# Kernel tuning notes

Hardware: AMD Instinct MI355X
Metric: run time of the kernel (lower is better)

Reference implementation:

```python
import jax, jax.numpy as jnp
import numpy as np

H, K, D = 24, 2, 128          # query heads, kv heads, head_size
HIDDEN = H * D                # 3072
ROPE_THETA = 10000.0


def setup_inputs() -> dict:
    key = jax.random.key(0)
    ks = jax.random.split(key, 6)
    B, S = 2, 2048
    T = B * S
    hidden_states = jax.random.normal(ks[0], (T, HIDDEN), dtype=jnp.float32)
    w_qkv = jax.random.normal(ks[1], ((H + 2 * K) * D, HIDDEN), dtype=jnp.float32) * (HIDDEN ** -0.5)
    b_qkv = jax.random.normal(ks[2], ((H + 2 * K) * D,), dtype=jnp.float32) * 0.02
    w_o = jax.random.normal(ks[3], (HIDDEN, H * D), dtype=jnp.float32) * (HIDDEN ** -0.5)
    b_o = jax.random.normal(ks[4], (HIDDEN,), dtype=jnp.float32) * 0.02
    # rotary tables: positions restart per sequence (flash-varlen prefill layout)
    pos = jnp.tile(jnp.arange(S, dtype=jnp.float32), B)            # [T]
    inv_freq = 1.0 / (ROPE_THETA ** (jnp.arange(0, D, 2, dtype=jnp.float32) / D))  # [D/2]
    freqs = pos[:, None] * inv_freq[None, :]                        # [T, D/2]
    return {
        "hidden_states": hidden_states,
        "w_qkv": w_qkv, "b_qkv": b_qkv,
        "w_o": w_o, "b_o": b_o,
        "cos": jnp.cos(freqs), "sin": jnp.sin(freqs),
        "seq_len": S, "window": 1024,
    }


def _rope(x, cos, sin):
    # rotate-half (neox) style, as in TGI PositionRotaryEmbedding
    half = x.shape[-1] // 2
    x1, x2 = x[..., :half], x[..., half:]
    c, s = cos[:, None, :], sin[:, None, :]   # broadcast over head dim
    return jnp.concatenate([x1 * c - x2 * s, x2 * c + x1 * s], axis=-1)


def reference(hidden_states, w_qkv, b_qkv, w_o, b_o, cos, sin, seq_len, window):
    T = hidden_states.shape[0]
    B = T // seq_len
    scale = D ** -0.5

    # fused QKV projection
    qkv = hidden_states @ w_qkv.T + b_qkv                 # [T, (H+2K)*D]
    q = qkv[:, : H * D].reshape(T, H, D)
    kv = qkv[:, H * D:].reshape(T, 2, K, D)
    k, v = kv[:, 0], kv[:, 1]                             # [T, K, D]

    q = _rope(q, cos, sin)
    k = _rope(k, cos, sin)

    # GQA: expand kv heads to query heads
    groups = H // K
    qb = q.reshape(B, seq_len, H, D)
    kb = jnp.repeat(k.reshape(B, seq_len, K, D), groups, axis=2)  # [B,S,H,D]
    vb = jnp.repeat(v.reshape(B, seq_len, K, D), groups, axis=2)

    scores = jnp.einsum("bqhd,bkhd->bhqk", qb, kb) * scale        # [B,H,S,S]
    idx = jnp.arange(seq_len)
    delta = idx[:, None] - idx[None, :]
    mask = (delta >= 0) & (delta < window)                        # causal + sliding window
    scores = jnp.where(mask[None, None], scores, jnp.float32(-1e9))
    attn = jax.nn.softmax(scores, axis=-1)
    out = jnp.einsum("bhqk,bkhd->bqhd", attn, vb).reshape(T, H * D)
    return out @ w_o.T + b_o
```

## Files before the change

### kernel.cpp

```cpp
#include <hip/hip_runtime.h>
#include <hip/hip_bf16.h>

typedef __attribute__((ext_vector_type(8))) short bf16x8;
typedef __attribute__((ext_vector_type(4))) float f32x4;

__device__ __forceinline__ short f2bf_bits(float f) {
    __hip_bfloat16 h = __float2bfloat16(f);
    short s;
    __builtin_memcpy(&s, &h, 2);
    return s;
}

__device__ __forceinline__ float bf_bits2f(short s) {
    unsigned int u = ((unsigned int)(unsigned short)s) << 16;
    float f;
    __builtin_memcpy(&f, &u, 4);
    return f;
}

__device__ __forceinline__ bf16x8 load8(const float* p) {
    float4 a = *(const float4*)p;
    float4 b = *(const float4*)(p + 4);
    bf16x8 r;
    r[0] = f2bf_bits(a.x); r[1] = f2bf_bits(a.y);
    r[2] = f2bf_bits(a.z); r[3] = f2bf_bits(a.w);
    r[4] = f2bf_bits(b.x); r[5] = f2bf_bits(b.y);
    r[6] = f2bf_bits(b.z); r[7] = f2bf_bits(b.w);
    return r;
}
__device__ __forceinline__ bf16x8 load8(const __hip_bfloat16* p) {
    return *(const bf16x8*)p;
}

__device__ __forceinline__ void store_out(__hip_bfloat16* p, float v) {
    *p = __float2bfloat16(v);
}
__device__ __forceinline__ void store_out(float* p, float v) { *p = v; }

__global__ void cvt3_f32_bf16(const float* __restrict__ a, short* __restrict__ da, int na8,
                              const float* __restrict__ b, short* __restrict__ db, int nb8,
                              const float* __restrict__ c, short* __restrict__ dc, int nc8) {
    int i = blockIdx.x * 256 + threadIdx.x;
    if (i < na8) {
        *(bf16x8*)(da + (size_t)i * 8) = load8(a + (size_t)i * 8);
    } else if ((i -= na8) < nb8) {
        *(bf16x8*)(db + (size_t)i * 8) = load8(b + (size_t)i * 8);
    } else if ((i -= nb8) < nc8) {
        *(bf16x8*)(dc + (size_t)i * 8) = load8(c + (size_t)i * 8);
    }
}

#define GB_REG 65536

__device__ __forceinline__ int half_off(int buf, int half) {
    return buf * 32768 + half * 16384;
}

template <typename TC>
__global__ __launch_bounds__(512) void gemm256(
    const __hip_bfloat16* __restrict__ A, const __hip_bfloat16* __restrict__ B,
    const float* __restrict__ bias, TC* __restrict__ C, int M, int N, int K)
{
    __shared__ char smem[131072];

    const int tid  = threadIdx.x;
    const int lane = tid & 63;
    const int wid  = tid >> 6;
    const int quad = lane >> 4;
    const int m16  = lane & 15;
    const int wmg  = wid >> 2;
    const int wng  = wid & 3;
    const int bhalf = wng >> 1;
    const int bsub  = (wng & 1) * 4;

    const int gx  = gridDim.x;
    const int nwg = gx * gridDim.y;
    int lin = blockIdx.y * gx + blockIdx.x;
    if ((nwg & 7) == 0) {
        int q = nwg >> 3;
        lin = (lin & 7) * q + (lin >> 3);
    }
    const int bn = lin % gx, bm = lin / gx;
    const int mBase = bm * 256, nBase = bn * 256;

    const int roff = (m16 << 6) | ((quad * 16) ^ ((m16 & 8) << 2));

    int r_s[2], c_s[2];
    #pragma unroll
    for (int l = 0; l < 2; ++l) {
        int sub = l * 8 + wid;
        int r16 = (tid >> 2) & 15;
        int cb  = ((tid & 3) * 16) ^ ((r16 & 8) << 2);
        r_s[l] = (sub >> 1) * 16 + r16;
        c_s[l] = (sub & 1) * 32 + (cb >> 1);
    }

    const __hip_bfloat16* Ab = A + (size_t)mBase * K;
    const __hip_bfloat16* Bb = B + (size_t)nBase * K;

    auto stage = [&](int region, const __hip_bfloat16* base, int buf, int half, int tile) {
        const __hip_bfloat16* gb = base + (size_t)(half * 128) * K + tile * 64;
        #pragma unroll
        for (int l = 0; l < 2; ++l) {
            const __hip_bfloat16* g = gb + (size_t)r_s[l] * K + c_s[l];
            short* lb = (short*)(smem + region + half_off(buf, half) + l * 8192 + wid * 1024);
            __builtin_amdgcn_global_load_lds(
                (__attribute__((address_space(1))) void*)g,
                (__attribute__((address_space(3))) void*)lb, 16, 0, 0);
        }
    };

    f32x4 acc[8][4] = {};
    bf16x8 afr[4][2];
    bf16x8 bfr[2][2][2];

    auto LD_A = [&](int buf, int g) {
        const char* base = smem + half_off(buf, wmg) + (g ? 8192 : 0);
        #pragma unroll
        for (int m = 0; m < 4; ++m)
            #pragma unroll
            for (int ks = 0; ks < 2; ++ks)
                afr[m][ks] = *(const bf16x8*)(base + ((m * 2 + ks) << 10) + roff);
    };
    auto LD_B = [&](int buf, int g) {
        const char* base = smem + GB_REG + half_off(buf, bhalf) + ((bsub + g * 2) << 11);
        #pragma unroll
        for (int j = 0; j < 2; ++j)
            #pragma unroll
            for (int ks = 0; ks < 2; ++ks)
                bfr[g][j][ks] = *(const bf16x8*)(base + ((j * 2 + ks) << 10) + roff);
    };
    auto MM = [&](int mo, int g) {
        #pragma unroll
        for (int m = 0; m < 4; ++m)
            #pragma unroll
            for (int j = 0; j < 2; ++j)
                #pragma unroll
                for (int ks = 0; ks < 2; ++ks)
                    acc[mo + m][g * 2 + j] = __builtin_amdgcn_mfma_f32_16x16x32_bf16(
                        afr[m][ks], bfr[g][j][ks], acc[mo + m][g * 2 + j], 0, 0, 0);
    };

#define SBAR() __builtin_amdgcn_s_barrier()
#define WAIT_LGKM0() do { asm volatile("s_waitcnt lgkmcnt(0)" ::: "memory"); \
                          __builtin_amdgcn_sched_barrier(0); } while (0)
#define WAIT_VM4()   do { asm volatile("s_waitcnt vmcnt(4)"   ::: "memory"); \
                          __builtin_amdgcn_sched_barrier(0); } while (0)

    const int NT = K >> 6;

    stage(GB_REG, Bb, 0, 0, 0);
    stage(0,      Ab, 0, 0, 0);
    stage(GB_REG, Bb, 0, 1, 0);
    stage(0,      Ab, 0, 1, 0);
    stage(GB_REG, Bb, 1, 0, 1);
    stage(0,      Ab, 1, 0, 1);
    WAIT_VM4();
    SBAR();

    for (int i = 0; i < (NT >> 1); ++i) {
        const int to = 2 * i + 1;
        const int t2 = min(2 * i + 2, NT - 1);
        const int t3 = min(2 * i + 3, NT - 1);
        LD_A(0, 0); LD_B(0, 0);
        stage(GB_REG, Bb, 1, 1, to);
        SBAR(); WAIT_LGKM0();
        __builtin_amdgcn_s_setprio(1); MM(0, 0); __builtin_amdgcn_s_setprio(0);
        SBAR();
        LD_B(0, 1);
        stage(0, Ab, 1, 1, to);
        SBAR(); WAIT_LGKM0();
        __builtin_amdgcn_s_setprio(1); MM(0, 1); __builtin_amdgcn_s_setprio(0);
        SBAR();
        LD_A(0, 1);
        stage(GB_REG, Bb, 0, 0, t2);
        SBAR(); WAIT_LGKM0();
        __builtin_amdgcn_s_setprio(1); MM(4, 1); __builtin_amdgcn_s_setprio(0);
        SBAR();
        stage(0, Ab, 0, 0, t2);
        WAIT_VM4();
        SBAR();
        __builtin_amdgcn_s_setprio(1); MM(4, 0); __builtin_amdgcn_s_setprio(0);
        SBAR();
        LD_A(1, 0); LD_B(1, 0);
        stage(GB_REG, Bb, 0, 1, t2);
        SBAR(); WAIT_LGKM0();
        __builtin_amdgcn_s_setprio(1); MM(0, 0); __builtin_amdgcn_s_setprio(0);
        SBAR();
        LD_B(1, 1);
        stage(0, Ab, 0, 1, t2);
        SBAR(); WAIT_LGKM0();
        __builtin_amdgcn_s_setprio(1); MM(0, 1); __builtin_amdgcn_s_setprio(0);
        SBAR();
        LD_A(1, 1);
        stage(GB_REG, Bb, 1, 0, t3);
        SBAR(); WAIT_LGKM0();
        __builtin_amdgcn_s_setprio(1); MM(4, 1); __builtin_amdgcn_s_setprio(0);
        SBAR();
        stage(0, Ab, 1, 0, t3);
        WAIT_VM4();
        SBAR();
        __builtin_amdgcn_s_setprio(1); MM(4, 0); __builtin_amdgcn_s_setprio(0);
        SBAR();
    }

#undef SBAR
#undef WAIT_LGKM0
#undef WAIT_VM4

    float bv[4];
    #pragma unroll
    for (int j = 0; j < 4; ++j)
        bv[j] = bias[nBase + wng * 64 + j * 16 + m16];

    #pragma unroll
    for (int mf = 0; mf < 8; ++mf) {
        #pragma unroll
        for (int j = 0; j < 4; ++j) {
            const int col = nBase + wng * 64 + j * 16 + m16;
            #pragma unroll
            for (int r = 0; r < 4; ++r) {
                const int row = mBase + wmg * 128 + mf * 16 + quad * 4 + r;
                store_out(&C[(size_t)row * N + col], acc[mf][j][r] + bv[j]);
            }
        }
    }
}

#define LDSS 40

template <typename TA, typename TB, typename TC>
__global__ __launch_bounds__(256) void gemm_bt_bias(
    const TA* __restrict__ A, const TB* __restrict__ B,
    const float* __restrict__ bias, TC* __restrict__ C, int M, int N, int K)
{
    __shared__ short As[128 * LDSS];
    __shared__ short Bs[128 * LDSS];

    const int tid  = threadIdx.x;
    const int lane = tid & 63;
    const int wid  = tid >> 6;
    const int quad = lane >> 4;
    const int m16  = lane & 15;

    const int mBase = blockIdx.y * 128;
    const int nBase = blockIdx.x * 128;
    const int wm = (wid >> 1) * 64;
    const int wn = (wid & 1) * 64;

    f32x4 acc[4][4] = {};
    const int srow = tid >> 2;
    const int sgrp = (tid & 3) * 8;

    for (int kt = 0; kt < K; kt += 32) {
        __syncthreads();
        for (int p = 0; p < 2; ++p) {
            int r = srow + p * 64;
            *(bf16x8*)(&As[r * LDSS + sgrp]) =
                load8(A + (size_t)(mBase + r) * K + kt + sgrp);
            *(bf16x8*)(&Bs[r * LDSS + sgrp]) =
                load8(B + (size_t)(nBase + r) * K + kt + sgrp);
        }
        __syncthreads();

        bf16x8 afr[4], bfr[4];
        #pragma unroll
        for (int i = 0; i < 4; ++i)
            afr[i] = *(const bf16x8*)(&As[(wm + 16 * i + m16) * LDSS + quad * 8]);
        #pragma unroll
        for (int j = 0; j < 4; ++j)
            bfr[j] = *(const bf16x8*)(&Bs[(wn + 16 * j + m16) * LDSS + quad * 8]);
        #pragma unroll
        for (int i = 0; i < 4; ++i)
            #pragma unroll
            for (int j = 0; j < 4; ++j)
                acc[i][j] = __builtin_amdgcn_mfma_f32_16x16x32_bf16(
                    afr[i], bfr[j], acc[i][j], 0, 0, 0);
    }

    float bv[4];
    #pragma unroll
    for (int j = 0; j < 4; ++j)
        bv[j] = bias[nBase + wn + 16 * j + m16];

    #pragma unroll
    for (int i = 0; i < 4; ++i)
        #pragma unroll
        for (int j = 0; j < 4; ++j) {
            int col = nBase + wn + 16 * j + m16;
            #pragma unroll
            for (int r = 0; r < 4; ++r) {
                int row = mBase + wm + 16 * i + quad * 4 + r;
                store_out(&C[(size_t)row * N + col], acc[i][j][r] + bv[j]);
            }
        }
}

__global__ void rope_kernel(__hip_bfloat16* __restrict__ qkv,
                            const float* __restrict__ cosb,
                            const float* __restrict__ sinb, int T)
{
    int idx = blockIdx.x * 256 + threadIdx.x;
    int total = T * 26 * 8;
    if (idx >= total) return;
    int j = idx & 7;
    int h = (idx >> 3) % 26;
    int t = idx / (26 * 8);
    int col = (h < 24) ? h * 128 : 3072 + (h - 24) * 128;
    int d0 = j * 8;
    size_t base = (size_t)t * 3584 + col + d0;
    bf16x8 x1 = *(const bf16x8*)((const short*)qkv + base);
    bf16x8 x2 = *(const bf16x8*)((const short*)qkv + base + 64);
    float4 c0 = *(const float4*)(cosb + t * 64 + d0);
    float4 c1 = *(const float4*)(cosb + t * 64 + d0 + 4);
    float4 s0 = *(const float4*)(sinb + t * 64 + d0);
    float4 s1 = *(const float4*)(sinb + t * 64 + d0 + 4);
    float cc[8] = {c0.x, c0.y, c0.z, c0.w, c1.x, c1.y, c1.z, c1.w};
    float ss[8] = {s0.x, s0.y, s0.z, s0.w, s1.x, s1.y, s1.z, s1.w};
    bf16x8 o1, o2;
    #pragma unroll
    for (int i = 0; i < 8; ++i) {
        float f1 = bf_bits2f(x1[i]);
        float f2 = bf_bits2f(x2[i]);
        o1[i] = f2bf_bits(f1 * cc[i] - f2 * ss[i]);
        o2[i] = f2bf_bits(f2 * cc[i] + f1 * ss[i]);
    }
    *(bf16x8*)((short*)qkv + base)      = o1;
    *(bf16x8*)((short*)qkv + base + 64) = o2;
}

#define SM_SHIFT 12.0f

__global__ __launch_bounds__(256, 3) void attn_kernel(
    const __hip_bfloat16* __restrict__ qkv,
    __hip_bfloat16* __restrict__ out,
    const int* __restrict__ seq_len_p, const int* __restrict__ window_p)
{
    const int S = seq_len_p[0];
    const int window = window_p[0];
    const float scale = 0.088388347648318447f;

    const int h   = blockIdx.y;
    const int kvh = h / 12;
    const int tid  = threadIdx.x;
    const int lane = tid & 63;
    const int wid  = tid >> 6;
    const int quad = lane >> 4;
    const int m16  = lane & 15;

    const int qb_global = blockIdx.x * 128;
    const int b  = qb_global / S;
    const int qb = qb_global - b * S;

    __shared__ short Vt[128 * 72];
    __shared__ short Ps[4][32 * 40];

    const size_t kvrow0 = (size_t)(b * S) * 3584 + 3072 + kvh * 128;

    bf16x8 qf[2][4];
    {
        const __hip_bfloat16* qp =
            qkv + (size_t)(qb_global + wid * 32 + m16) * 3584 + h * 128;
        #pragma unroll
        for (int qt = 0; qt < 2; ++qt)
            #pragma unroll
            for (int dc = 0; dc < 4; ++dc)
                qf[qt][dc] = *(const bf16x8*)(qp + qt * 16 * 3584 + dc * 32 + quad * 8);
    }

    f32x4 accO[2][8] = {};
    float lqt[2] = {0.f, 0.f};

    int ka0 = qb - window + 1;
    if (ka0 < 0) ka0 = 0;
    ka0 &= ~31;
    const int kend = qb + 128;

    for (int kt = ka0; kt < kend; kt += 32) {
        __syncthreads();
        #pragma unroll
        for (int p = 0; p < 2; ++p) {
            int L   = tid + p * 256;
            int key = L & 31;
            int gg  = L >> 5;
            int d0  = gg * 8;
            bf16x8 v8 = *(const bf16x8*)(qkv + kvrow0 + (size_t)(kt + key) * 3584 + 256 + d0);
            short* dst = &Vt[d0 * 72 + key + (gg & 1) * 32];
            #pragma unroll
            for (int i2 = 0; i2 < 8; ++i2) dst[i2 * 72] = v8[i2];
        }
        __syncthreads();

        f32x4 sacc[2][2] = {};
        #pragma unroll
        for (int st = 0; st < 2; ++st) {
            const __hip_bfloat16* kp =
                qkv + kvrow0 + (size_t)(kt + st * 16 + m16) * 3584;
            #pragma unroll
            for (int dc = 0; dc < 4; ++dc) {
                bf16x8 kf = *(const bf16x8*)(kp + dc * 32 + quad * 8);
                sacc[st][0] = __builtin_amdgcn_mfma_f32_16x16x32_bf16(
                    kf, qf[0][dc], sacc[st][0], 0, 0, 0);
                sacc[st][1] = __builtin_amdgcn_mfma_f32_16x16x32_bf16(
                    kf, qf[1][dc], sacc[st][1], 0, 0, 0);
            }
        }

        #pragma unroll
        for (int qt = 0; qt < 2; ++qt) {
            const int qmin = qb + wid * 32 + qt * 16;
            short* prow = &Ps[wid][(qt * 16 + m16) * 40];
            float psum = 0.f;
            if (kt <= qmin - 31 && kt >= qmin + 16 - window) {
                #pragma unroll
                for (int st = 0; st < 2; ++st)
                    #pragma unroll
                    for (int r = 0; r < 4; ++r) {
                        float pp = __expf(fminf(
                            sacc[st][qt][r] * scale - SM_SHIFT, 80.f));
                        psum += pp;
                        prow[st * 16 + quad * 4 + r] = f2bf_bits(pp);
                    }
            } else {
                const int dl_base = (qmin + m16) - (kt + quad * 4);
                #pragma unroll
                for (int st = 0; st < 2; ++st)
                    #pragma unroll
                    for (int r = 0; r < 4; ++r) {
                        int dl = dl_base - st * 16 - r;
                        float pp = ((unsigned)dl < (unsigned)window)
                            ? __expf(fminf(sacc[st][qt][r] * scale - SM_SHIFT, 80.f))
                            : 0.f;
                        psum += pp;
                        prow[st * 16 + quad * 4 + r] = f2bf_bits(pp);
                    }
            }
            psum += __shfl_xor(psum, 16, 64);
            psum += __shfl_xor(psum, 32, 64);
            lqt[qt] += psum;
        }

        bf16x8 pf0 = *(const bf16x8*)(&Ps[wid][(0  + m16) * 40 + quad * 8]);
        bf16x8 pf1 = *(const bf16x8*)(&Ps[wid][(16 + m16) * 40 + quad * 8]);
        #pragma unroll
        for (int dt = 0; dt < 8; ++dt) {
            int row = dt * 16 + m16;
            bf16x8 vf = *(const bf16x8*)(&Vt[row * 72 + quad * 8 + ((row >> 3) & 1) * 32]);
            accO[0][dt] = __builtin_amdgcn_mfma_f32_16x16x32_bf16(pf0, vf, accO[0][dt], 0, 0, 0);
            accO[1][dt] = __builtin_amdgcn_mfma_f32_16x16x32_bf16(pf1, vf, accO[1][dt], 0, 0, 0);
        }
    }

    #pragma unroll
    for (int qt = 0; qt < 2; ++qt) {
        float li[4];
        #pragma unroll
        for (int r = 0; r < 4; ++r)
            li[r] = 1.0f / __shfl(lqt[qt], quad * 4 + r, 64);
        #pragma unroll
        for (int r = 0; r < 4; ++r) {
            int t = qb_global + wid * 32 + qt * 16 + quad * 4 + r;
            __hip_bfloat16* op = out + (size_t)t * 3072 + h * 128 + m16;
            #pragma unroll
            for (int dt = 0; dt < 8; ++dt)
                op[dt * 16] = __float2bfloat16(accO[qt][dt][r] * li[r]);
        }
    }
}

extern "C" void kernel_launch(void* const* d_in, const int* in_sizes, int n_in,
                              void* d_out, int out_size, void* d_ws, size_t ws_size,
                              hipStream_t stream) {
    const float* hidden = (const float*)d_in[0];
    const float* w_qkv  = (const float*)d_in[1];
    const float* b_qkv  = (const float*)d_in[2];
    const float* w_o    = (const float*)d_in[3];
    const float* b_o    = (const float*)d_in[4];
    const float* cosb   = (const float*)d_in[5];
    const float* sinb   = (const float*)d_in[6];
    const int* seq_len_p = (const int*)d_in[7];
    const int* window_p  = (const int*)d_in[8];

    const int HID  = in_sizes[4];
    const int NQKV = in_sizes[2];
    const int T    = in_sizes[0] / HID;

    size_t off = 0;
    auto alloc = [&](size_t bytes) {
        char* p = (char*)d_ws + off;
        off = (off + bytes + 255) & ~(size_t)255;
        return p;
    };
    __hip_bfloat16* qkv      = (__hip_bfloat16*)alloc((size_t)T * NQKV * 2);
    __hip_bfloat16* attn_out = (__hip_bfloat16*)alloc((size_t)T * HID * 2);
    __hip_bfloat16* hid_bf = (__hip_bfloat16*)alloc((size_t)T * HID * 2);
    __hip_bfloat16* wq_bf  = (__hip_bfloat16*)alloc((size_t)NQKV * HID * 2);
    __hip_bfloat16* wo_bf  = (__hip_bfloat16*)alloc((size_t)HID * HID * 2);
    const bool pre = (ws_size >= off);
    const bool big = pre && (T % 256 == 0) && (NQKV % 256 == 0) &&
                     (HID % 256 == 0) && (HID % 64 == 0);

    dim3 blk(256);

    if (big) {
        int n8h = T * HID / 8, n8q = NQKV * HID / 8, n8o = HID * HID / 8;
        int n8 = n8h + n8q + n8o;
        cvt3_f32_bf16<<<dim3((n8 + 255) / 256), blk, 0, stream>>>(
            hidden, (short*)hid_bf, n8h, w_qkv, (short*)wq_bf, n8q,
            w_o, (short*)wo_bf, n8o);
        gemm256<__hip_bfloat16><<<dim3(NQKV / 256, T / 256), dim3(512), 0, stream>>>(
            hid_bf, wq_bf, b_qkv, qkv, T, NQKV, HID);
    } else {
        gemm_bt_bias<float, float, __hip_bfloat16>
            <<<dim3(NQKV / 128, T / 128), blk, 0, stream>>>(
            hidden, w_qkv, b_qkv, qkv, T, NQKV, HID);
    }

    int total = T * 26 * 8;
    rope_kernel<<<dim3((total + 255) / 256), blk, 0, stream>>>(qkv, cosb, sinb, T);

    attn_kernel<<<dim3(T / 128, 24), blk, 0, stream>>>(qkv, attn_out, seq_len_p, window_p);

    if (big) {
        gemm256<float><<<dim3(HID / 256, T / 256), dim3(512), 0, stream>>>(
            attn_out, wo_bf, b_o, (float*)d_out, T, HID, HID);
    } else {
        gemm_bt_bias<__hip_bfloat16, float, float>
            <<<dim3(HID / 128, T / 128), blk, 0, stream>>>(
            attn_out, w_o, b_o, (float*)d_out, T, HID, HID);
    }
}
```

Before: 479.5 us.

## Change LDS swizzle, reverse query-block order, prefetch V before barrier, add setprio

The GEMM LDS swizzle changes from a single-bit XOR to a two-bit XOR across row pairs, aimed at fewer bank conflicts. The attention kernel now maps blocks so the heaviest query blocks (highest positions, most keys) launch first, which evens out the tail of the launch. Inside the key loop, V global loads are issued before the first barrier so they overlap the wait, and raw s_barrier calls with an explicit lgkmcnt wait replace __syncthreads. The PV MFMA section also runs at raised wave priority. The hand-placed barriers and waitcnt risk missing a vmcnt ordering, and the swizzle change has to stay consistent between the store and read paths.

```diff
diff --git a/kernel.cpp b/kernel.cpp
--- a/kernel.cpp
+++ b/kernel.cpp
@@ -83,14 +83,14 @@
     const int bn = lin % gx, bm = lin / gx;
     const int mBase = bm * 256, nBase = bn * 256;
 
-    const int roff = (m16 << 6) | ((quad * 16) ^ ((m16 & 8) << 2));
+    const int roff = (m16 << 6) | ((quad * 16) ^ (((m16 >> 1) & 3) << 4));
 
     int r_s[2], c_s[2];
     #pragma unroll
     for (int l = 0; l < 2; ++l) {
         int sub = l * 8 + wid;
         int r16 = (tid >> 2) & 15;
-        int cb  = ((tid & 3) * 16) ^ ((r16 & 8) << 2);
+        int cb  = ((tid & 3) * 16) ^ (((r16 >> 1) & 3) << 4);
         r_s[l] = (sub >> 1) * 16 + r16;
         c_s[l] = (sub & 1) * 32 + (cb >> 1);
     }
@@ -348,9 +348,11 @@
     const int quad = lane >> 4;
     const int m16  = lane & 15;
 
-    const int qb_global = blockIdx.x * 128;
-    const int b  = qb_global / S;
-    const int qb = qb_global - b * S;
+    const int nbb = S >> 7;
+    const int b   = blockIdx.x / nbb;
+    const int ib  = blockIdx.x - b * nbb;
+    const int qb  = (nbb - 1 - ib) << 7;
+    const int qb_global = b * S + qb;
 
     __shared__ short Vt[128 * 72];
     __shared__ short Ps[4][32 * 40];
@@ -375,21 +377,31 @@
     if (ka0 < 0) ka0 = 0;
     ka0 &= ~31;
     const int kend = qb + 128;
-
-    for (int kt = ka0; kt < kend; kt += 32) {
-        __syncthreads();
-        #pragma unroll
-        for (int p = 0; p < 2; ++p) {
-            int L   = tid + p * 256;
-            int key = L & 31;
-            int gg  = L >> 5;
-            int d0  = gg * 8;
-            bf16x8 v8 = *(const bf16x8*)(qkv + kvrow0 + (size_t)(kt + key) * 3584 + 256 + d0);
-            short* dst = &Vt[d0 * 72 + key + (gg & 1) * 32];
-            #pragma unroll
-            for (int i2 = 0; i2 < 8; ++i2) dst[i2 * 72] = v8[i2];
-        }
-        __syncthreads();
+    const int niter = (kend - ka0) >> 5;
+
+    const int skey = tid & 31;
+    const int sgg0 = tid >> 5;
+    const int sgg1 = sgg0 + 8;
+
+    for (int it = 0; it < niter; ++it) {
+        const int kt = ka0 + it * 32;
+
+        bf16x8 v0 = *(const bf16x8*)(qkv + kvrow0 + (size_t)(kt + skey) * 3584 + 256 + sgg0 * 8);
+        bf16x8 v1 = *(const bf16x8*)(qkv + kvrow0 + (size_t)(kt + skey) * 3584 + 256 + sgg1 * 8);
+
+        __builtin_amdgcn_s_barrier();
+
+        {
+            short* dst0 = &Vt[(sgg0 * 8) * 72 + skey + (sgg0 & 1) * 32];
+            short* dst1 = &Vt[(sgg1 * 8) * 72 + skey + (sgg1 & 1) * 32];
+            #pragma unroll
+            for (int i2 = 0; i2 < 8; ++i2) dst0[i2 * 72] = v0[i2];
+            #pragma unroll
+            for (int i2 = 0; i2 < 8; ++i2) dst1[i2 * 72] = v1[i2];
+        }
+        asm volatile("s_waitcnt lgkmcnt(0)" ::: "memory");
+        __builtin_amdgcn_s_barrier();
+        __builtin_amdgcn_sched_barrier(0);
 
         f32x4 sacc[2][2] = {};
         #pragma unroll
@@ -442,6 +454,7 @@
 
         bf16x8 pf0 = *(const bf16x8*)(&Ps[wid][(0  + m16) * 40 + quad * 8]);
         bf16x8 pf1 = *(const bf16x8*)(&Ps[wid][(16 + m16) * 40 + quad * 8]);
+        __builtin_amdgcn_s_setprio(1);
         #pragma unroll
         for (int dt = 0; dt < 8; ++dt) {
             int row = dt * 16 + m16;
@@ -449,6 +462,7 @@
             accO[0][dt] = __builtin_amdgcn_mfma_f32_16x16x32_bf16(pf0, vf, accO[0][dt], 0, 0, 0);
             accO[1][dt] = __builtin_amdgcn_mfma_f32_16x16x32_bf16(pf1, vf, accO[1][dt], 0, 0, 0);
         }
+        __builtin_amdgcn_s_setprio(0);
     }
 
     #pragma unroll
```

New measurement: 480.7 us. About the same (+0.3%).
